# Kernel tuning notes

Hardware: AMD Instinct MI355X
Metric: run time of the kernel (lower is better)

The kernel has to match this reference:

```python
import jax, jax.numpy as jnp
import numpy as np

NUM_BINS = 256
EPS = 1e-08


def setup_inputs() -> dict:
    key = jax.random.key(0)
    k1, k2 = jax.random.split(key)
    B, C, H, W = 16, 3, 512, 512
    pred = jax.random.uniform(k1, (B, C, H, W), dtype=jnp.float32)
    target = jax.random.uniform(k2, (B, C, H, W), dtype=jnp.float32)
    return {"pred": pred, "target": target}


def _compute_histogram(x):
    """Per-(batch, channel) 256-bin histogram of values in [0, 1].

    Faithful to torch.histc(bins=N, min=0, max=1): bin width 1/N,
    value v -> bin floor(v*N), with v == 1.0 landing in the last bin
    (handled by the clip). Values outside [0,1] are ignored.
    Implemented as a single fused scatter-add over all B*C histograms.
    """
    B, C, H, W = x.shape
    in_range = (x >= 0.0) & (x <= 1.0)
    bins = jnp.clip(jnp.floor(x * NUM_BINS).astype(jnp.int32), 0, NUM_BINS - 1)
    # flat index into [B*C, NUM_BINS] histogram array
    bc = jnp.arange(B * C, dtype=jnp.int32)[:, None]  # [B*C, 1]
    flat_idx = (bc * NUM_BINS + bins.reshape(B * C, H * W)).reshape(-1)
    weights = in_range.reshape(-1).astype(x.dtype)
    hist = jnp.zeros(B * C * NUM_BINS, dtype=x.dtype).at[flat_idx].add(weights)
    return hist.reshape(B, C, NUM_BINS)


def reference(pred, target):
    pred_hist = _compute_histogram(pred)
    target_hist = _compute_histogram(target)
    pred_hist = pred_hist / (pred_hist.sum(axis=2, keepdims=True) + EPS)
    target_hist = target_hist / (target_hist.sum(axis=2, keepdims=True) + EPS)
    return jnp.mean((pred_hist - target_hist) ** 2)
```

## Files before the change

### kernel.cpp

```cpp
#include <hip/hip_runtime.h>

#define NUM_BINS 256
#define PLANES 48
#define PLANE_ELEMS (512 * 512)
#define BPP 16
#define THREADS 256
#define F4_PER_BLOCK (PLANE_ELEMS / 4 / BPP)
#define F4_PER_THREAD (F4_PER_BLOCK / THREADS)
#define NSUB 8
#define HSTRIDE 257
#define BATCH 4

__global__ __launch_bounds__(THREADS) void hist_kernel(const float* __restrict__ pred,
                                                       const float* __restrict__ target,
                                                       unsigned* __restrict__ part) {
    __shared__ alignas(16) unsigned lh[NSUB * HSTRIDE];
    const int t = threadIdx.x;
    const int lane = t & 63;

    uint4* l4 = reinterpret_cast<uint4*>(lh);
    for (int i = t; i < (NSUB * HSTRIDE + 3) / 4; i += THREADS) l4[i] = make_uint4(0, 0, 0, 0);
    __syncthreads();

    const int gid   = blockIdx.x;
    const int which = gid / (PLANES * BPP);
    const int rem   = gid - which * (PLANES * BPP);
    const int plane = rem / BPP;
    const int cblk  = rem - plane * BPP;

    const float* src = which ? target : pred;
    const float4* p = reinterpret_cast<const float4*>(src + (size_t)plane * PLANE_ELEMS)
                      + (size_t)cblk * F4_PER_BLOCK;

    unsigned* sub = lh + (size_t)(lane & (NSUB - 1)) * HSTRIDE;

    float4 cur[BATCH], nxt[BATCH];
#pragma unroll
    for (int j = 0; j < BATCH; ++j) cur[j] = p[j * THREADS + t];

    for (int c = 0; c < F4_PER_THREAD / BATCH; ++c) {
        if (c + 1 < F4_PER_THREAD / BATCH) {
#pragma unroll
            for (int j = 0; j < BATCH; ++j)
                nxt[j] = p[(c + 1) * BATCH * THREADS + j * THREADS + t];
        }
#pragma unroll
        for (int j = 0; j < BATCH; ++j) {
            float e[4] = {cur[j].x, cur[j].y, cur[j].z, cur[j].w};
#pragma unroll
            for (int k = 0; k < 4; ++k) {
                int b = (int)(e[k] * 256.0f);
                b = b > 255 ? 255 : b;
                atomicAdd(&sub[b], 1u);
            }
        }
#pragma unroll
        for (int j = 0; j < BATCH; ++j) cur[j] = nxt[j];
    }
    __syncthreads();

    unsigned c = 0;
#pragma unroll
    for (int h = 0; h < NSUB; ++h) c += lh[h * HSTRIDE + t];
    part[(size_t)gid * NUM_BINS + t] = c;
}

__global__ __launch_bounds__(THREADS) void plane_kernel(const unsigned* __restrict__ part,
                                                        double* __restrict__ plane_loss) {
    __shared__ unsigned wa[4], wb[4];
    __shared__ double sd[THREADS];
    const int t = threadIdx.x;
    const int p = blockIdx.x;

    const unsigned* bp = part + (size_t)p * BPP * NUM_BINS;
    const unsigned* bt = part + (size_t)(PLANES + p) * BPP * NUM_BINS;
    unsigned hp = 0, ht = 0;
#pragma unroll
    for (int j = 0; j < BPP; ++j) {
        hp += bp[j * NUM_BINS + t];
        ht += bt[j * NUM_BINS + t];
    }

    unsigned a = hp, b = ht;
    for (int off = 32; off; off >>= 1) {
        a += __shfl_down(a, off, 64);
        b += __shfl_down(b, off, 64);
    }
    if ((t & 63) == 0) { wa[t >> 6] = a; wb[t >> 6] = b; }
    __syncthreads();
    const unsigned Sp = wa[0] + wa[1] + wa[2] + wa[3];
    const unsigned St = wb[0] + wb[1] + wb[2] + wb[3];

    const double ip = 1.0 / ((double)Sp + 1e-8);
    const double it = 1.0 / ((double)St + 1e-8);
    const double d = (double)hp * ip - (double)ht * it;
    sd[t] = d * d;
    __syncthreads();
    for (int off = THREADS / 2; off; off >>= 1) {
        if (t < off) sd[t] += sd[t + off];
        __syncthreads();
    }
    if (t == 0) plane_loss[p] = sd[0];
}

__global__ __launch_bounds__(64) void final_kernel(const double* __restrict__ plane_loss,
                                                   float* __restrict__ out) {
    const int t = threadIdx.x;
    double v = (t < PLANES) ? plane_loss[t] : 0.0;
    for (int off = 32; off; off >>= 1) v += __shfl_down(v, off, 64);
    if (t == 0) out[0] = (float)(v / (double)(PLANES * NUM_BINS));
}

extern "C" void kernel_launch(void* const* d_in, const int* in_sizes, int n_in,
                              void* d_out, int out_size, void* d_ws, size_t ws_size,
                              hipStream_t stream) {
    const float* pred   = (const float*)d_in[0];
    const float* target = (const float*)d_in[1];
    float* out = (float*)d_out;
    unsigned* part = (unsigned*)d_ws;
    double* plane_loss = reinterpret_cast<double*>(
        (char*)d_ws + (size_t)2 * PLANES * BPP * NUM_BINS * sizeof(unsigned));

    hist_kernel<<<2 * PLANES * BPP, THREADS, 0, stream>>>(pred, target, part);
    plane_kernel<<<PLANES, THREADS, 0, stream>>>(part, plane_loss);
    final_kernel<<<1, 64, 0, stream>>>(plane_loss, out);
}
```

Measured before the change: 24.84 us.

## Mix LDS atomic histogramming with wave ballot-based bin counting

Half of each thread's data is still binned with LDS atomics. The other half is counted with wavefront ballots: eight ballots over the bin bits let each lane count the matches for its own four bins with popcounts, and each lane then adds those counts with four atomics. The goal is to spread the work between the LDS atomic pipe and the scalar/VALU ballot path so they overlap. The ballot path costs many extra instructions per element and assumes exactly 16 float4 loads per thread.

```diff
diff --git a/kernel.cpp b/kernel.cpp
--- a/kernel.cpp
+++ b/kernel.cpp
@@ -6,7 +6,6 @@
 #define BPP 16
 #define THREADS 256
 #define F4_PER_BLOCK (PLANE_ELEMS / 4 / BPP)
-#define F4_PER_THREAD (F4_PER_BLOCK / THREADS)
 #define NSUB 8
 #define HSTRIDE 257
 #define BATCH 4
@@ -34,29 +33,81 @@
 
     unsigned* sub = lh + (size_t)(lane & (NSUB - 1)) * HSTRIDE;
 
-    float4 cur[BATCH], nxt[BATCH];
+    const unsigned m0 = ((lane >> 0) & 1) ? 0u : ~0u;
+    const unsigned m1 = ((lane >> 1) & 1) ? 0u : ~0u;
+    const unsigned m2 = ((lane >> 2) & 1) ? 0u : ~0u;
+    const unsigned m3 = ((lane >> 3) & 1) ? 0u : ~0u;
+    const unsigned m4 = ((lane >> 4) & 1) ? 0u : ~0u;
+    const unsigned m5 = ((lane >> 5) & 1) ? 0u : ~0u;
+    unsigned c0 = 0, c1 = 0, c2 = 0, c3 = 0;
+
+#define ATOMIC4(v)                                                                \
+    do {                                                                          \
+        float e_[4] = {(v).x, (v).y, (v).z, (v).w};                               \
+        _Pragma("unroll")                                                         \
+        for (int k_ = 0; k_ < 4; ++k_) {                                          \
+            int b_ = (int)(e_[k_] * 256.0f);   \
+            b_ = b_ > 255 ? 255 : b_;                        \
+            atomicAdd(&sub[b_], 1u);                   \
+        }                                                                         \
+    } while (0)
+
+#define ROUND(xx)                                                                 \
+    do {                                                                          \
+        float x = (xx);                                                           \
+        int b = (int)(x * 256.0f);                                                \
+        b = b > 255 ? 255 : b;                                                    \
+        unsigned long long B1 = __ballot(b & 2);                                  \
+        unsigned long long B2 = __ballot(b & 4);                                  \
+        unsigned long long B3 = __ballot(b & 8);                                  \
+        unsigned long long B4 = __ballot(b & 16);                                 \
+        unsigned long long B5 = __ballot(b & 32);                                 \
+        unsigned long long B6 = __ballot(b & 64);                                 \
+        unsigned long long B0 = __ballot(b & 1);                                  \
+        unsigned long long B7 = __ballot(b & 128);                                \
+        unsigned long long Te0 = ~B0 & ~B7, Te1 = B0 & ~B7;                       \
+        unsigned long long Te2 = ~B0 &  B7, Te3 = B0 &  B7;                       \
+        unsigned lo = ((unsigned)B1 ^ m0) & ((unsigned)B2 ^ m1) &                 \
+                      ((unsigned)B3 ^ m2) & ((unsigned)B4 ^ m3) &                 \
+                      ((unsigned)B5 ^ m4) & ((unsigned)B6 ^ m5);                  \
+        unsigned hi = ((unsigned)(B1 >> 32) ^ m0) & ((unsigned)(B2 >> 32) ^ m1) & \
+                      ((unsigned)(B3 >> 32) ^ m2) & ((unsigned)(B4 >> 32) ^ m3) & \
+                      ((unsigned)(B5 >> 32) ^ m4) & ((unsigned)(B6 >> 32) ^ m5);  \
+        c0 += __popc(lo & (unsigned)Te0) + __popc(hi & (unsigned)(Te0 >> 32));    \
+        c1 += __popc(lo & (unsigned)Te1) + __popc(hi & (unsigned)(Te1 >> 32));    \
+        c2 += __popc(lo & (unsigned)Te2) + __popc(hi & (unsigned)(Te2 >> 32));    \
+        c3 += __popc(lo & (unsigned)Te3) + __popc(hi & (unsigned)(Te3 >> 32));    \
+    } while (0)
+
+#define BALLOT4(v) do { ROUND((v).x); ROUND((v).y); ROUND((v).z); ROUND((v).w); } while (0)
+
+    float4 vA[BATCH], vB[BATCH], vC[BATCH], vD[BATCH];
 #pragma unroll
-    for (int j = 0; j < BATCH; ++j) cur[j] = p[j * THREADS + t];
+    for (int j = 0; j < BATCH; ++j) vA[j] = p[(0 * BATCH + j) * THREADS + t];
+#pragma unroll
+    for (int j = 0; j < BATCH; ++j) vB[j] = p[(1 * BATCH + j) * THREADS + t];
 
-    for (int c = 0; c < F4_PER_THREAD / BATCH; ++c) {
-        if (c + 1 < F4_PER_THREAD / BATCH) {
 #pragma unroll
-            for (int j = 0; j < BATCH; ++j)
-                nxt[j] = p[(c + 1) * BATCH * THREADS + j * THREADS + t];
-        }
+    for (int j = 0; j < BATCH; ++j) ATOMIC4(vA[j]);
 #pragma unroll
-        for (int j = 0; j < BATCH; ++j) {
-            float e[4] = {cur[j].x, cur[j].y, cur[j].z, cur[j].w};
+    for (int j = 0; j < BATCH; ++j) vC[j] = p[(2 * BATCH + j) * THREADS + t];
 #pragma unroll
-            for (int k = 0; k < 4; ++k) {
-                int b = (int)(e[k] * 256.0f);
-                b = b > 255 ? 255 : b;
-                atomicAdd(&sub[b], 1u);
-            }
-        }
+    for (int j = 0; j < BATCH; ++j) BALLOT4(vB[j]);
 #pragma unroll
-        for (int j = 0; j < BATCH; ++j) cur[j] = nxt[j];
-    }
+    for (int j = 0; j < BATCH; ++j) vD[j] = p[(3 * BATCH + j) * THREADS + t];
+#pragma unroll
+    for (int j = 0; j < BATCH; ++j) ATOMIC4(vC[j]);
+#pragma unroll
+    for (int j = 0; j < BATCH; ++j) BALLOT4(vD[j]);
+
+#undef BALLOT4
+#undef ROUND
+#undef ATOMIC4
+
+    atomicAdd(&sub[2 * lane], c0);
+    atomicAdd(&sub[2 * lane + 1], c1);
+    atomicAdd(&sub[128 + 2 * lane], c2);
+    atomicAdd(&sub[129 + 2 * lane], c3);
     __syncthreads();
 
     unsigned c = 0;
```

New measurement: 32.71 us. 1.32x slower.
